# Kernel optimization log

Measured on AMD Instinct MI355X. Metric: run time of the kernel, lower is better.

Reference implementation:

```python
import jax, jax.numpy as jnp
import numpy as np

N_NODES = 50000
N_EDGES = 800000
D = 96

def setup_inputs() -> dict:
    key = jax.random.key(0)
    ks = jax.random.split(key, 8)
    g = 0.1  # glorot-ish scale
    return {
        "x": jax.random.normal(ks[0], (N_NODES, D), jnp.float32),
        "edge_index": jax.random.randint(ks[1], (2, N_EDGES), 0, N_NODES, jnp.int64),
        "W1_root": jax.random.normal(ks[2], (D, D), jnp.float32) * g,
        "W1_nbr": jax.random.normal(ks[3], (D, D), jnp.float32) * g,
        "b1": jnp.zeros((D,), jnp.float32),
        "W2_root": jax.random.normal(ks[4], (D, D), jnp.float32) * g,
        "W2_nbr": jax.random.normal(ks[5], (D, D), jnp.float32) * g,
        "b2": jnp.zeros((D,), jnp.float32),
        "lin_w": jax.random.normal(ks[6], (D, 2 * D), jnp.float32) * g,
        "lin_b": jnp.zeros((D,), jnp.float32),
    }

def _conv(h, src, dst, W_root, W_nbr, b, neighbor_norm):
    # gather messages from source nodes, scatter-add into destination nodes
    agg = jax.ops.segment_sum(h[src], dst, num_segments=N_NODES)  # [N, D]
    if neighbor_norm:
        deg = jax.ops.segment_sum(jnp.ones_like(dst, dtype=h.dtype), dst,
                                  num_segments=N_NODES)
        agg = agg / jnp.maximum(deg, 1.0)[:, None]
    return h @ W_root + agg @ W_nbr + b

def reference(x, edge_index, W1_root, W1_nbr, b1, W2_root, W2_nbr, b2, lin_w, lin_b):
    src, dst = edge_index[0], edge_index[1]
    h1 = _conv(x, src, dst, W1_root, W1_nbr, b1, neighbor_norm=False)  # conv1, norm='None'
    h2 = _conv(h1, src, dst, W2_root, W2_nbr, b2, neighbor_norm=True)  # conv, neighbornorm
    # dropout is identity in eval mode; out=False so no global pooling
    cat = jnp.concatenate([h1, h2], axis=-1)  # [N, 2D]
    return jax.nn.relu(cat @ lin_w.T + lin_b)
```

## Files before the change

kernel.cpp:

```cpp
#include <hip/hip_runtime.h>

#define DN 96
#define NCHUNK 256

typedef __attribute__((ext_vector_type(8))) short bf16x8;
typedef __attribute__((ext_vector_type(4))) float f32x4;

__device__ __forceinline__ int edge_at(const void* ei, long long idx, int use64) {
    if (use64) return (int)((const long long*)ei)[idx];
    return ((const int*)ei)[idx];
}

__device__ __forceinline__ unsigned short f2bf(float f) {
    unsigned int u = __float_as_uint(f);
    return (unsigned short)((u + 0x7fffu + ((u >> 16) & 1u)) >> 16);
}

__global__ void detect_i64(const unsigned int* w, int* flagp) {
    __shared__ int ok;
    if (threadIdx.x == 0) ok = 1;
    __syncthreads();
    for (int i = threadIdx.x; i < 1024; i += blockDim.x)
        if (w[2 * i + 1] != 0u) ok = 0;
    __syncthreads();
    if (threadIdx.x == 0) flagp[0] = ok;
}

__global__ void preprocess(const float* __restrict__ x, unsigned int* __restrict__ xb,
                           const void* __restrict__ ei, const int* __restrict__ flagp,
                           unsigned int* __restrict__ eidx,
                           const float* __restrict__ W1r, const float* __restrict__ W1n,
                           const float* __restrict__ W2r, const float* __restrict__ W2n,
                           const float* __restrict__ lw, unsigned short* __restrict__ WT,
                           long long E, int NP) {
    int use64 = flagp[0];
    long long total = (long long)NP + E + 3LL * DN * 192;
    long long stride = (long long)gridDim.x * blockDim.x;
    for (long long i = (long long)blockIdx.x * blockDim.x + threadIdx.x; i < total; i += stride) {
        if (i < NP) {
            float2 v = *(const float2*)(x + 2 * i);
            xb[i] = (unsigned int)f2bf(v.x) | ((unsigned int)f2bf(v.y) << 16);
        } else if (i < NP + E) {
            long long e = i - NP;
            int s = edge_at(ei, e, use64);
            int d = edge_at(ei, E + e, use64);
            eidx[e] = (unsigned int)s | ((unsigned int)d << 16);
        } else {
            long long j = i - NP - E;
            int w = (int)(j / (DN * 192));
            int r = (int)(j % (DN * 192));
            int jj = r / 192, k = r % 192;
            float v;
            if (w == 0)      v = (k < DN) ? W1r[(size_t)k * DN + jj] : W1n[(size_t)(k - DN) * DN + jj];
            else if (w == 1) v = (k < DN) ? W2r[(size_t)k * DN + jj] : W2n[(size_t)(k - DN) * DN + jj];
            else             v = lw[r];
            WT[j] = f2bf(v);
        }
    }
}

__global__ void hist_chunks(const unsigned int* __restrict__ eidx, long long E,
                            int* __restrict__ hist, int nbuck, long long CE) {
    __shared__ int lh[800];
    int c = blockIdx.x, tid = threadIdx.x;
    for (int b = tid; b < nbuck; b += 256) lh[b] = 0;
    __syncthreads();
    long long beg = (long long)c * CE;
    long long end = beg + CE; if (end > E) end = E;
    for (long long e = beg + tid; e < end; e += 256) {
        unsigned int u = eidx[e];
        atomicAdd(&lh[(u >> 16) >> 6], 1);
    }
    __syncthreads();
    for (int b = tid; b < nbuck; b += 256)
        hist[(size_t)c * nbuck + b] = lh[b];
}

__global__ void bucket_tot(const int* __restrict__ hist, int* __restrict__ btot,
                           int nbuck) {
    __shared__ int ws[4];
    int b = blockIdx.x, tid = threadIdx.x;
    int lane = tid & 63, wid = tid >> 6;
    int v = hist[(size_t)tid * nbuck + b];
#pragma unroll
    for (int off = 32; off >= 1; off >>= 1) v += __shfl_down(v, off, 64);
    if (lane == 0) ws[wid] = v;
    __syncthreads();
    if (tid == 0) btot[b] = ws[0] + ws[1] + ws[2] + ws[3];
}

__global__ void scan_excl(int* data, int n) {
    __shared__ int swsum[16];
    int tid = threadIdx.x;
    int lane = tid & 63, wid = tid >> 6;
    int carry = 0;
    for (int base = 0; base < n; base += 1024) {
        int i = base + tid;
        int v = (i < n) ? data[i] : 0;
        int sv = v;
#pragma unroll
        for (int off = 1; off < 64; off <<= 1) {
            int t = __shfl_up(sv, off, 64);
            if (lane >= off) sv += t;
        }
        __syncthreads();
        if (lane == 63) swsum[wid] = sv;
        __syncthreads();
        if (tid < 16) {
            int wv = swsum[tid];
#pragma unroll
            for (int off = 1; off < 16; off <<= 1) {
                int t = __shfl_up(wv, off, 16);
                if (tid >= off) wv += t;
            }
            swsum[tid] = wv;
        }
        __syncthreads();
        int woff = (wid > 0) ? swsum[wid - 1] : 0;
        int excl = carry + woff + sv - v;
        if (i < n) data[i] = excl;
        carry += swsum[15];
        __syncthreads();
    }
    if (tid == 0) data[n] = carry;
}

__global__ void chunk_scan(const int* __restrict__ hist, const int* __restrict__ bstart,
                           int* __restrict__ pos, int nbuck) {
    __shared__ int wsum[4];
    int b = blockIdx.x, tid = threadIdx.x;
    int lane = tid & 63, wid = tid >> 6;
    int v = hist[(size_t)tid * nbuck + b];
    int sv = v;
#pragma unroll
    for (int off = 1; off < 64; off <<= 1) {
        int t = __shfl_up(sv, off, 64);
        if (lane >= off) sv += t;
    }
    if (lane == 63) wsum[wid] = sv;
    __syncthreads();
    int woff = 0;
    for (int w = 0; w < wid; ++w) woff += wsum[w];
    pos[(size_t)tid * nbuck + b] = bstart[b] + woff + sv - v;
}

__global__ void scatter_grouped(const unsigned int* __restrict__ eidx, long long E,
                                const int* __restrict__ pos,
                                unsigned int* __restrict__ packed,
                                int nbuck, long long CE) {
    __shared__ int cur[800];
    int c = blockIdx.x, tid = threadIdx.x;
    for (int b = tid; b < nbuck; b += 256) cur[b] = pos[(size_t)c * nbuck + b];
    __syncthreads();
    long long beg = (long long)c * CE;
    long long end = beg + CE; if (end > E) end = E;
    for (long long e = beg + tid; e < end; e += 256) {
        unsigned int u = eidx[e];
        int src = (int)(u & 0xFFFFu);
        int dst = (int)(u >> 16);
        int b = dst >> 6;
        int p = atomicAdd(&cur[b], 1);
        packed[p] = (unsigned int)src | ((unsigned int)(dst & 63) << 16);
    }
}

__global__ void bucket_sort(const unsigned int* __restrict__ packed,
                            const int* __restrict__ bstart,
                            unsigned short* __restrict__ csr_src,
                            int* __restrict__ rowptr, int n, int nbuck) {
    __shared__ int bin[64];
    __shared__ int cur[64];
    int b = blockIdx.x, tid = threadIdx.x;
    int beg = bstart[b], end = bstart[b + 1];
    if (tid < 64) bin[tid] = 0;
    __syncthreads();
    for (int i = beg + tid; i < end; i += 256)
        atomicAdd(&bin[packed[i] >> 16], 1);
    __syncthreads();
    if (tid < 64) {
        int v = bin[tid];
        int sv = v;
#pragma unroll
        for (int off = 1; off < 64; off <<= 1) {
            int t = __shfl_up(sv, off, 64);
            if (tid >= off) sv += t;
        }
        int excl = sv - v;
        cur[tid] = beg + excl;
        int node = b * 64 + tid;
        if (node < n) rowptr[node] = beg + excl;
    }
    __syncthreads();
    for (int i = beg + tid; i < end; i += 256) {
        unsigned int p = packed[i];
        int q = atomicAdd(&cur[p >> 16], 1);
        csr_src[q] = (unsigned short)(p & 0xFFFFu);
    }
    if (b == nbuck - 1 && tid == 0) rowptr[n] = end;
}

__global__ void aggregate(const unsigned int* __restrict__ in, unsigned int* __restrict__ out,
                          const int* __restrict__ rowptr,
                          const unsigned short* __restrict__ srcs,
                          int n, int normalize) {
    int t = blockIdx.x * blockDim.x + threadIdx.x;
    if (t >= n * 12) return;
    int node = t / 12, c = t % 12;
    int beg = rowptr[node], end = rowptr[node + 1];
    float acc[8];
#pragma unroll
    for (int j = 0; j < 8; ++j) acc[j] = 0.f;
    for (int i = beg; i < end; ++i) {
        int s = srcs[i];
        const uint4 v = *(const uint4*)(in + (size_t)s * 48 + c * 4);
        unsigned int u;
        u = v.x; acc[0] += __uint_as_float(u << 16); acc[1] += __uint_as_float(u & 0xffff0000u);
        u = v.y; acc[2] += __uint_as_float(u << 16); acc[3] += __uint_as_float(u & 0xffff0000u);
        u = v.z; acc[4] += __uint_as_float(u << 16); acc[5] += __uint_as_float(u & 0xffff0000u);
        u = v.w; acc[6] += __uint_as_float(u << 16); acc[7] += __uint_as_float(u & 0xffff0000u);
    }
    if (normalize) {
        float inv = 1.0f / fmaxf((float)(end - beg), 1.0f);
#pragma unroll
        for (int j = 0; j < 8; ++j) acc[j] *= inv;
    }
    uint4 r;
    r.x = (unsigned int)f2bf(acc[0]) | ((unsigned int)f2bf(acc[1]) << 16);
    r.y = (unsigned int)f2bf(acc[2]) | ((unsigned int)f2bf(acc[3]) << 16);
    r.z = (unsigned int)f2bf(acc[4]) | ((unsigned int)f2bf(acc[5]) << 16);
    r.w = (unsigned int)f2bf(acc[6]) | ((unsigned int)f2bf(acc[7]) << 16);
    *(uint4*)(out + (size_t)node * 48 + c * 4) = r;
}

__global__ __launch_bounds__(256) void gemm_mfma(
        const unsigned short* __restrict__ Abf, const unsigned short* __restrict__ Bbf,
        const unsigned short* __restrict__ WT, const float* __restrict__ bias,
        float* __restrict__ outf, unsigned short* __restrict__ outb,
        int n, int dorelu) {
    __shared__ unsigned int WTl[DN * 100];
    int tid = threadIdx.x;
    const unsigned int* WTg = (const unsigned int*)WT;
    for (int i = tid; i < DN * 96; i += 256) {
        int j = i / 96, m = i - j * 96;
        WTl[j * 100 + m] = WTg[i];
    }
    __syncthreads();

    int wid = tid >> 6, lane = tid & 63;
    int lg = lane >> 4, lr = lane & 15;
    int rowbase = blockIdx.x * 128 + wid * 32;

    f32x4 acc[2][6];
#pragma unroll
    for (int rt = 0; rt < 2; ++rt)
#pragma unroll
        for (int ct = 0; ct < 6; ++ct) acc[rt][ct] = (f32x4){0.f, 0.f, 0.f, 0.f};

    const unsigned short* WTs = (const unsigned short*)WTl;
#pragma unroll
    for (int kt = 0; kt < 6; ++kt) {
        const unsigned short* src = (kt < 3) ? Abf : Bbf;
        int kk = (kt < 3 ? kt : kt - 3) * 32 + lg * 8;
        bf16x8 afrag[2];
#pragma unroll
        for (int rt = 0; rt < 2; ++rt) {
            int row = rowbase + rt * 16 + lr;
            if (row >= n) row = n - 1;
            afrag[rt] = *(const bf16x8*)(src + (size_t)row * DN + kk);
        }
        int koff = kt * 32 + lg * 8;
#pragma unroll
        for (int ct = 0; ct < 6; ++ct) {
            bf16x8 bfrag = *(const bf16x8*)(WTs + (ct * 16 + lr) * 200 + koff);
            acc[0][ct] = __builtin_amdgcn_mfma_f32_16x16x32_bf16(afrag[0], bfrag, acc[0][ct], 0, 0, 0);
            acc[1][ct] = __builtin_amdgcn_mfma_f32_16x16x32_bf16(afrag[1], bfrag, acc[1][ct], 0, 0, 0);
        }
    }

#pragma unroll
    for (int ct = 0; ct < 6; ++ct) {
        int col = ct * 16 + lr;
        float bv = bias[col];
#pragma unroll
        for (int rt = 0; rt < 2; ++rt)
#pragma unroll
            for (int r = 0; r < 4; ++r) {
                int row = rowbase + rt * 16 + lg * 4 + r;
                if (row < n) {
                    float v = acc[rt][ct][r] + bv;
                    if (dorelu) v = fmaxf(v, 0.f);
                    if (outf) outf[(size_t)row * DN + col] = v;
                    if (outb) outb[(size_t)row * DN + col] = f2bf(v);
                }
            }
    }
}

__global__ __launch_bounds__(256) void gemm_fused(
        const unsigned short* __restrict__ h1, const unsigned short* __restrict__ agg,
        const unsigned short* __restrict__ WT2, const float* __restrict__ b2,
        const unsigned short* __restrict__ WT3, const float* __restrict__ lb,
        float* __restrict__ out, int n) {
    __shared__ unsigned int WTl[DN * 100];
    __shared__ unsigned short h2t[4][32][98];
    int tid = threadIdx.x, wid = tid >> 6, lane = tid & 63;
    int lg = lane >> 4, lr = lane & 15;
    int rowbase = blockIdx.x * 128 + wid * 32;

    const unsigned int* WTg2 = (const unsigned int*)WT2;
    for (int i = tid; i < DN * 96; i += 256) {
        int j = i / 96, m = i - j * 96;
        WTl[j * 100 + m] = WTg2[i];
    }
    __syncthreads();

    f32x4 acc[2][6];
#pragma unroll
    for (int rt = 0; rt < 2; ++rt)
#pragma unroll
        for (int ct = 0; ct < 6; ++ct) acc[rt][ct] = (f32x4){0.f, 0.f, 0.f, 0.f};

    const unsigned short* WTs = (const unsigned short*)WTl;
    bf16x8 afragA[2][3];
#pragma unroll
    for (int kt = 0; kt < 6; ++kt) {
        bf16x8 afrag[2];
#pragma unroll
        for (int rt = 0; rt < 2; ++rt) {
            int row = rowbase + rt * 16 + lr;
            if (row >= n) row = n - 1;
            if (kt < 3) {
                afrag[rt] = *(const bf16x8*)(h1 + (size_t)row * DN + kt * 32 + lg * 8);
                afragA[rt][kt] = afrag[rt];
            } else {
                afrag[rt] = *(const bf16x8*)(agg + (size_t)row * DN + (kt - 3) * 32 + lg * 8);
            }
        }
        int koff = kt * 32 + lg * 8;
#pragma unroll
        for (int ct = 0; ct < 6; ++ct) {
            bf16x8 bfrag = *(const bf16x8*)(WTs + (ct * 16 + lr) * 200 + koff);
            acc[0][ct] = __builtin_amdgcn_mfma_f32_16x16x32_bf16(afrag[0], bfrag, acc[0][ct], 0, 0, 0);
            acc[1][ct] = __builtin_amdgcn_mfma_f32_16x16x32_bf16(afrag[1], bfrag, acc[1][ct], 0, 0, 0);
        }
    }

#pragma unroll
    for (int ct = 0; ct < 6; ++ct) {
        float bv = b2[ct * 16 + lr];
#pragma unroll
        for (int rt = 0; rt < 2; ++rt)
#pragma unroll
            for (int r = 0; r < 4; ++r)
                h2t[wid][rt * 16 + lg * 4 + r][ct * 16 + lr] = f2bf(acc[rt][ct][r] + bv);
    }
    __syncthreads();

    const unsigned int* WTg3 = (const unsigned int*)WT3;
    for (int i = tid; i < DN * 96; i += 256) {
        int j = i / 96, m = i - j * 96;
        WTl[j * 100 + m] = WTg3[i];
    }
    __syncthreads();

    f32x4 acc2[2][6];
#pragma unroll
    for (int rt = 0; rt < 2; ++rt)
#pragma unroll
        for (int ct = 0; ct < 6; ++ct) acc2[rt][ct] = (f32x4){0.f, 0.f, 0.f, 0.f};

#pragma unroll
    for (int kt = 0; kt < 6; ++kt) {
        bf16x8 afrag[2];
#pragma unroll
        for (int rt = 0; rt < 2; ++rt) {
            if (kt < 3) afrag[rt] = afragA[rt][kt];
            else        afrag[rt] = *(const bf16x8*)(&h2t[wid][rt * 16 + lr][(kt - 3) * 32 + lg * 8]);
        }
        int koff = kt * 32 + lg * 8;
#pragma unroll
        for (int ct = 0; ct < 6; ++ct) {
            bf16x8 bfrag = *(const bf16x8*)(WTs + (ct * 16 + lr) * 200 + koff);
            acc2[0][ct] = __builtin_amdgcn_mfma_f32_16x16x32_bf16(afrag[0], bfrag, acc2[0][ct], 0, 0, 0);
            acc2[1][ct] = __builtin_amdgcn_mfma_f32_16x16x32_bf16(afrag[1], bfrag, acc2[1][ct], 0, 0, 0);
        }
    }

#pragma unroll
    for (int ct = 0; ct < 6; ++ct) {
        int col = ct * 16 + lr;
        float bv = lb[col];
#pragma unroll
        for (int rt = 0; rt < 2; ++rt)
#pragma unroll
            for (int r = 0; r < 4; ++r) {
                int row = rowbase + rt * 16 + lg * 4 + r;
                if (row < n)
                    out[(size_t)row * DN + col] = fmaxf(acc2[rt][ct][r] + bv, 0.f);
            }
    }
}

extern "C" void kernel_launch(void* const* d_in, const int* in_sizes, int n_in,
                              void* d_out, int out_size, void* d_ws, size_t ws_size,
                              hipStream_t stream) {
    const float* x   = (const float*)d_in[0];
    const void*  ei  = d_in[1];
    const float* W1r = (const float*)d_in[2];
    const float* W1n = (const float*)d_in[3];
    const float* b1  = (const float*)d_in[4];
    const float* W2r = (const float*)d_in[5];
    const float* W2n = (const float*)d_in[6];
    const float* b2  = (const float*)d_in[7];
    const float* lw  = (const float*)d_in[8];
    const float* lb  = (const float*)d_in[9];
    float* out = (float*)d_out;

    const int N = in_sizes[0] / DN;
    const long long E = in_sizes[1] / 2;
    const int NBUCK = (N + 63) / 64;
    const long long CE = (E + NCHUNK - 1) / NCHUNK;
    const size_t NP = (size_t)N * 48;

    unsigned int* xb   = (unsigned int*)d_ws;
    unsigned int* h1b  = xb + NP;
    unsigned int* aggb = h1b + NP;
    unsigned short* WT = (unsigned short*)(aggb + NP);
    unsigned short* WT1 = WT;
    unsigned short* WT2 = WT + DN * 192;
    unsigned short* WT3 = WT2 + DN * 192;
    unsigned int* eidx = (unsigned int*)(WT3 + DN * 192);
    int* hist   = (int*)(eidx + E);
    int* pos    = hist + NCHUNK * NBUCK;
    int* btot   = pos + NCHUNK * NBUCK;
    int* rowptr = btot + NBUCK + 1;
    unsigned int* packed = (unsigned int*)(rowptr + N + 1);
    unsigned short* csr_src = (unsigned short*)(packed + E);
    int* flagp  = (int*)(csr_src + E);

    detect_i64<<<1, 256, 0, stream>>>((const unsigned int*)ei, flagp);
    preprocess<<<4096, 256, 0, stream>>>(x, xb, ei, flagp, eidx,
                                         W1r, W1n, W2r, W2n, lw, WT, E, (int)NP);

    hist_chunks<<<NCHUNK, 256, 0, stream>>>(eidx, E, hist, NBUCK, CE);
    bucket_tot<<<NBUCK, 256, 0, stream>>>(hist, btot, NBUCK);
    scan_excl<<<1, 1024, 0, stream>>>(btot, NBUCK);
    chunk_scan<<<NBUCK, 256, 0, stream>>>(hist, btot, pos, NBUCK);
    scatter_grouped<<<NCHUNK, 256, 0, stream>>>(eidx, E, pos, packed, NBUCK, CE);
    bucket_sort<<<NBUCK, 256, 0, stream>>>(packed, btot, csr_src, rowptr, N, NBUCK);

    int ab = (N * 12 + 255) / 256;
    int gb = (N + 127) / 128;

    aggregate<<<ab, 256, 0, stream>>>(xb, aggb, rowptr, csr_src, N, 0);
    gemm_mfma<<<gb, 256, 0, stream>>>((const unsigned short*)xb, (const unsigned short*)aggb,
                                      WT1, b1, (float*)0, (unsigned short*)h1b, N, 0);
    aggregate<<<ab, 256, 0, stream>>>(h1b, aggb, rowptr, csr_src, N, 1);
    gemm_fused<<<gb, 256, 0, stream>>>((const unsigned short*)h1b, (const unsigned short*)aggb,
                                       WT2, b2, WT3, lb, out, N);
}
```

Before: 152.3 us.

## Fuse preprocessing, int64 detection and histogram; merge bucket scans; unroll aggregation

```diff
diff --git a/kernel.cpp b/kernel.cpp
--- a/kernel.cpp
+++ b/kernel.cpp
@@ -16,77 +16,73 @@
     return (unsigned short)((u + 0x7fffu + ((u >> 16) & 1u)) >> 16);
 }
 
-__global__ void detect_i64(const unsigned int* w, int* flagp) {
-    __shared__ int ok;
-    if (threadIdx.x == 0) ok = 1;
-    __syncthreads();
-    for (int i = threadIdx.x; i < 1024; i += blockDim.x)
-        if (w[2 * i + 1] != 0u) ok = 0;
-    __syncthreads();
-    if (threadIdx.x == 0) flagp[0] = ok;
-}
-
-__global__ void preprocess(const float* __restrict__ x, unsigned int* __restrict__ xb,
-                           const void* __restrict__ ei, const int* __restrict__ flagp,
-                           unsigned int* __restrict__ eidx,
-                           const float* __restrict__ W1r, const float* __restrict__ W1n,
-                           const float* __restrict__ W2r, const float* __restrict__ W2n,
-                           const float* __restrict__ lw, unsigned short* __restrict__ WT,
-                           long long E, int NP) {
-    int use64 = flagp[0];
-    long long total = (long long)NP + E + 3LL * DN * 192;
-    long long stride = (long long)gridDim.x * blockDim.x;
-    for (long long i = (long long)blockIdx.x * blockDim.x + threadIdx.x; i < total; i += stride) {
-        if (i < NP) {
-            float2 v = *(const float2*)(x + 2 * i);
-            xb[i] = (unsigned int)f2bf(v.x) | ((unsigned int)f2bf(v.y) << 16);
-        } else if (i < NP + E) {
-            long long e = i - NP;
-            int s = edge_at(ei, e, use64);
-            int d = edge_at(ei, E + e, use64);
-            eidx[e] = (unsigned int)s | ((unsigned int)d << 16);
-        } else {
-            long long j = i - NP - E;
-            int w = (int)(j / (DN * 192));
-            int r = (int)(j % (DN * 192));
-            int jj = r / 192, k = r % 192;
-            float v;
-            if (w == 0)      v = (k < DN) ? W1r[(size_t)k * DN + jj] : W1n[(size_t)(k - DN) * DN + jj];
-            else if (w == 1) v = (k < DN) ? W2r[(size_t)k * DN + jj] : W2n[(size_t)(k - DN) * DN + jj];
-            else             v = lw[r];
-            WT[j] = f2bf(v);
-        }
-    }
-}
-
-__global__ void hist_chunks(const unsigned int* __restrict__ eidx, long long E,
-                            int* __restrict__ hist, int nbuck, long long CE) {
+__global__ __launch_bounds__(256) void preprocess(
+        const float* __restrict__ x, unsigned int* __restrict__ xb,
+        const void* __restrict__ ei, unsigned int* __restrict__ eidx,
+        int* __restrict__ hist,
+        const float* __restrict__ W1r, const float* __restrict__ W1n,
+        const float* __restrict__ W2r, const float* __restrict__ W2n,
+        const float* __restrict__ lw, unsigned short* __restrict__ WT,
+        long long E, long long CE, int nbuck, int NP) {
     __shared__ int lh[800];
+    __shared__ int flag;
     int c = blockIdx.x, tid = threadIdx.x;
+
+    if (tid == 0) flag = 1;
     for (int b = tid; b < nbuck; b += 256) lh[b] = 0;
     __syncthreads();
+    if (((const unsigned int*)ei)[2 * tid + 1] != 0u) atomicAnd(&flag, 0);
+    __syncthreads();
+    int use64 = flag;
+
     long long beg = (long long)c * CE;
     long long end = beg + CE; if (end > E) end = E;
     for (long long e = beg + tid; e < end; e += 256) {
-        unsigned int u = eidx[e];
-        atomicAdd(&lh[(u >> 16) >> 6], 1);
+        int s = edge_at(ei, e, use64);
+        int d = edge_at(ei, E + e, use64);
+        eidx[e] = (unsigned int)s | ((unsigned int)d << 16);
+        atomicAdd(&lh[d >> 6], 1);
     }
     __syncthreads();
     for (int b = tid; b < nbuck; b += 256)
         hist[(size_t)c * nbuck + b] = lh[b];
-}
-
-__global__ void bucket_tot(const int* __restrict__ hist, int* __restrict__ btot,
-                           int nbuck) {
-    __shared__ int ws[4];
+
+    int gstride = gridDim.x * 256;
+    for (int i = c * 256 + tid; i < NP; i += gstride) {
+        float2 v = *(const float2*)(x + 2 * (size_t)i);
+        xb[i] = (unsigned int)f2bf(v.x) | ((unsigned int)f2bf(v.y) << 16);
+    }
+
+    for (int j = c * 256 + tid; j < 3 * DN * 192; j += gstride) {
+        int w = j / (DN * 192);
+        int r = j % (DN * 192);
+        int jj = r / 192, k = r % 192;
+        float v;
+        if (w == 0)      v = (k < DN) ? W1r[(size_t)k * DN + jj] : W1n[(size_t)(k - DN) * DN + jj];
+        else if (w == 1) v = (k < DN) ? W2r[(size_t)k * DN + jj] : W2n[(size_t)(k - DN) * DN + jj];
+        else             v = lw[r];
+        WT[j] = f2bf(v);
+    }
+}
+
+__global__ void bucket_scan(const int* __restrict__ hist, int* __restrict__ pos_rel,
+                            int* __restrict__ btot, int nbuck) {
+    __shared__ int wsum[4];
     int b = blockIdx.x, tid = threadIdx.x;
     int lane = tid & 63, wid = tid >> 6;
     int v = hist[(size_t)tid * nbuck + b];
-#pragma unroll
-    for (int off = 32; off >= 1; off >>= 1) v += __shfl_down(v, off, 64);
-    if (lane == 0) ws[wid] = v;
-    __syncthreads();
-    if (tid == 0) btot[b] = ws[0] + ws[1] + ws[2] + ws[3];
+    int sv = v;
+#pragma unroll
+    for (int off = 1; off < 64; off <<= 1) {
+        int t = __shfl_up(sv, off, 64);
+        if (lane >= off) sv += t;
+    }
+    if (lane == 63) wsum[wid] = sv;
+    __syncthreads();
+    int woff = 0;
+    for (int w = 0; w < wid; ++w) woff += wsum[w];
+    pos_rel[(size_t)tid * nbuck + b] = woff + sv - v;
+    if (tid == 255) btot[b] = woff + sv;
 }
 
 __global__ void scan_excl(int* data, int n) {
@@ -125,32 +121,15 @@
     if (tid == 0) data[n] = carry;
 }
 
-__global__ void chunk_scan(const int* __restrict__ hist, const int* __restrict__ bstart,
-                           int* __restrict__ pos, int nbuck) {
-    __shared__ int wsum[4];
-    int b = blockIdx.x, tid = threadIdx.x;
-    int lane = tid & 63, wid = tid >> 6;
-    int v = hist[(size_t)tid * nbuck + b];
-    int sv = v;
-#pragma unroll
-    for (int off = 1; off < 64; off <<= 1) {
-        int t = __shfl_up(sv, off, 64);
-        if (lane >= off) sv += t;
-    }
-    if (lane == 63) wsum[wid] = sv;
-    __syncthreads();
-    int woff = 0;
-    for (int w = 0; w < wid; ++w) woff += wsum[w];
-    pos[(size_t)tid * nbuck + b] = bstart[b] + woff + sv - v;
-}
-
 __global__ void scatter_grouped(const unsigned int* __restrict__ eidx, long long E,
-                                const int* __restrict__ pos,
+                                const int* __restrict__ pos_rel,
+                                const int* __restrict__ bstart,
                                 unsigned int* __restrict__ packed,
                                 int nbuck, long long CE) {
     __shared__ int cur[800];
     int c = blockIdx.x, tid = threadIdx.x;
-    for (int b = tid; b < nbuck; b += 256) cur[b] = pos[(size_t)c * nbuck + b];
+    for (int b = tid; b < nbuck; b += 256)
+        cur[b] = pos_rel[(size_t)c * nbuck + b] + bstart[b];
     __syncthreads();
     long long beg = (long long)c * CE;
     long long end = beg + CE; if (end > E) end = E;
@@ -199,6 +178,14 @@
     if (b == nbuck - 1 && tid == 0) rowptr[n] = end;
 }
 
+__device__ __forceinline__ void acc_row(float* acc, uint4 v) {
+    unsigned int u;
+    u = v.x; acc[0] += __uint_as_float(u << 16); acc[1] += __uint_as_float(u & 0xffff0000u);
+    u = v.y; acc[2] += __uint_as_float(u << 16); acc[3] += __uint_as_float(u & 0xffff0000u);
+    u = v.z; acc[4] += __uint_as_float(u << 16); acc[5] += __uint_as_float(u & 0xffff0000u);
+    u = v.w; acc[6] += __uint_as_float(u << 16); acc[7] += __uint_as_float(u & 0xffff0000u);
+}
+
 __global__ void aggregate(const unsigned int* __restrict__ in, unsigned int* __restrict__ out,
                           const int* __restrict__ rowptr,
                           const unsigned short* __restrict__ srcs,
@@ -210,14 +197,18 @@
     float acc[8];
 #pragma unroll
     for (int j = 0; j < 8; ++j) acc[j] = 0.f;
-    for (int i = beg; i < end; ++i) {
-        int s = srcs[i];
-        const uint4 v = *(const uint4*)(in + (size_t)s * 48 + c * 4);
-        unsigned int u;
-        u = v.x; acc[0] += __uint_as_float(u << 16); acc[1] += __uint_as_float(u & 0xffff0000u);
-        u = v.y; acc[2] += __uint_as_float(u << 16); acc[3] += __uint_as_float(u & 0xffff0000u);
-        u = v.z; acc[4] += __uint_as_float(u << 16); acc[5] += __uint_as_float(u & 0xffff0000u);
-        u = v.w; acc[6] += __uint_as_float(u << 16); acc[7] += __uint_as_float(u & 0xffff0000u);
+    int i = beg;
+    for (; i + 4 <= end; i += 4) {
+        int s0 = srcs[i], s1 = srcs[i + 1], s2 = srcs[i + 2], s3 = srcs[i + 3];
+        uint4 v0 = *(const uint4*)(in + (size_t)s0 * 48 + c * 4);
+        uint4 v1 = *(const uint4*)(in + (size_t)s1 * 48 + c * 4);
+        uint4 v2 = *(const uint4*)(in + (size_t)s2 * 48 + c * 4);
+        uint4 v3 = *(const uint4*)(in + (size_t)s3 * 48 + c * 4);
+        acc_row(acc, v0); acc_row(acc, v1); acc_row(acc, v2); acc_row(acc, v3);
+    }
+    for (; i < end; ++i) {
+        uint4 v = *(const uint4*)(in + (size_t)srcs[i] * 48 + c * 4);
+        acc_row(acc, v);
     }
     if (normalize) {
         float inv = 1.0f / fmaxf((float)(end - beg), 1.0f);
@@ -436,17 +427,13 @@
     int* rowptr = btot + NBUCK + 1;
     unsigned int* packed = (unsigned int*)(rowptr + N + 1);
     unsigned short* csr_src = (unsigned short*)(packed + E);
-    int* flagp  = (int*)(csr_src + E);
-
-    detect_i64<<<1, 256, 0, stream>>>((const unsigned int*)ei, flagp);
-    preprocess<<<4096, 256, 0, stream>>>(x, xb, ei, flagp, eidx,
-                                         W1r, W1n, W2r, W2n, lw, WT, E, (int)NP);
-
-    hist_chunks<<<NCHUNK, 256, 0, stream>>>(eidx, E, hist, NBUCK, CE);
-    bucket_tot<<<NBUCK, 256, 0, stream>>>(hist, btot, NBUCK);
+
+    preprocess<<<NCHUNK, 256, 0, stream>>>(x, xb, ei, eidx, hist,
+                                           W1r, W1n, W2r, W2n, lw, WT,
+                                           E, CE, NBUCK, (int)NP);
+    bucket_scan<<<NBUCK, 256, 0, stream>>>(hist, pos, btot, NBUCK);
     scan_excl<<<1, 1024, 0, stream>>>(btot, NBUCK);
-    chunk_scan<<<NBUCK, 256, 0, stream>>>(hist, btot, pos, NBUCK);
-    scatter_grouped<<<NCHUNK, 256, 0, stream>>>(eidx, E, pos, packed, NBUCK, CE);
+    scatter_grouped<<<NCHUNK, 256, 0, stream>>>(eidx, E, pos, btot, packed, NBUCK, CE);
     bucket_sort<<<NBUCK, 256, 0, stream>>>(packed, btot, csr_src, rowptr, N, NBUCK);
 
     int ab = (N * 12 + 255) / 256;
```

Result: faster. 123.9 us (-18.6%).
